# Optimization experiments

Hardware: AMD Instinct MI355X
Metric: run time of the kernel (lower is better)

## Reference

```python
import jax, jax.numpy as jnp
import numpy as np

N = 100000   # nodes
E = 400000   # edges (before self-loops)
G = 4000     # graphs in batch
F_IN = 32    # node_embedding
HID = 128    # hidden_channels
H = 3        # heads (hard-coded in module)
W3 = H * HID # 384, post-concat width
NC = 10      # num_classes
NL = 4       # num_layers
NEG_SLOPE = 0.2


def _lin(key, fan_in, fan_out):
    return jax.random.normal(key, (fan_in, fan_out), jnp.float32) * (1.0 / np.sqrt(fan_in))


def setup_inputs() -> dict:
    key = jax.random.key(0)
    ks = iter(jax.random.split(key, 40))
    x = jax.random.normal(next(ks), (N, F_IN), jnp.float32)
    edge_index = jax.random.randint(next(ks), (2, E), 0, N, dtype=jnp.int32)
    batch = jnp.sort(jax.random.randint(next(ks), (N,), 0, G, dtype=jnp.int32))
    inp = dict(x=x, edge_index=edge_index, batch=batch)
    # MLP stem
    inp['lin1_w'] = _lin(next(ks), F_IN, 2 * HID); inp['lin1_b'] = jnp.zeros((2 * HID,), jnp.float32)
    inp['lin2_w'] = _lin(next(ks), 2 * HID, HID);  inp['lin2_b'] = jnp.zeros((HID,), jnp.float32)
    # conv1: GATConv(HID -> HID, heads=3)
    inp['w0'] = _lin(next(ks), HID, W3)
    inp['as0'] = jax.random.normal(next(ks), (H, HID), jnp.float32) * 0.1
    inp['ad0'] = jax.random.normal(next(ks), (H, HID), jnp.float32) * 0.1
    inp['b0'] = jnp.zeros((W3,), jnp.float32)
    # remaining NL-1 convs: GATConv(W3 -> HID, heads=3), stacked
    inp['wl'] = jnp.stack([_lin(next(ks), W3, W3) for _ in range(NL - 1)])
    inp['asl'] = jax.random.normal(next(ks), (NL - 1, H, HID), jnp.float32) * 0.1
    inp['adl'] = jax.random.normal(next(ks), (NL - 1, H, HID), jnp.float32) * 0.1
    inp['bl'] = jnp.zeros((NL - 1, W3), jnp.float32)
    # batch norms (NL total, all width W3)
    inp['gamma'] = jnp.ones((NL, W3), jnp.float32)
    inp['beta'] = jnp.zeros((NL, W3), jnp.float32)
    # head
    inp['lin3_w'] = _lin(next(ks), W3, HID); inp['lin3_b'] = jnp.zeros((HID,), jnp.float32)
    inp['lin4_w'] = _lin(next(ks), HID, NC); inp['lin4_b'] = jnp.zeros((NC,), jnp.float32)
    return inp


def _gat(x, W, a_src, a_dst, bias, src, dst):
    # PyG GATConv, concat heads. x: [N, Fin]
    h = (x @ W).reshape(N, H, HID)                       # [N, H, C]
    es = jnp.einsum('nhc,hc->nh', h, a_src)              # [N, H]
    ed = jnp.einsum('nhc,hc->nh', h, a_dst)
    e = jax.nn.leaky_relu(es[src] + ed[dst], NEG_SLOPE)  # [Etot, H]
    m = jax.ops.segment_max(e, dst, num_segments=N)      # segment softmax over incoming edges
    p = jnp.exp(e - m[dst])
    s = jax.ops.segment_sum(p, dst, num_segments=N)
    alpha = p / s[dst]                                   # every node has a self-loop -> s>0
    out = jax.ops.segment_sum(alpha[:, :, None] * h[src], dst, num_segments=N)
    return out.reshape(N, W3) + bias


def _bn(x, g, b):
    mu = x.mean(0)
    var = x.var(0)
    return (x - mu) * jax.lax.rsqrt(var + 1e-5) * g + b


def reference(x, edge_index, batch, lin1_w, lin1_b, lin2_w, lin2_b,
              w0, as0, ad0, b0, wl, asl, adl, bl, gamma, beta,
              lin3_w, lin3_b, lin4_w, lin4_b):
    loop = jnp.arange(N, dtype=edge_index.dtype)
    src = jnp.concatenate([edge_index[0], loop])  # add_self_loops=True (PyG default)
    dst = jnp.concatenate([edge_index[1], loop])
    h = jax.nn.relu(x @ lin1_w + lin1_b)
    h = jax.nn.relu(h @ lin2_w + lin2_b)
    h = _gat(h, w0, as0, ad0, b0, src, dst)
    h = _bn(h, gamma[0], beta[0])
    for i in range(NL - 1):
        h = _gat(h, wl[i], asl[i], adl[i], bl[i], src, dst)
        h = _bn(h, gamma[i + 1], beta[i + 1])
    # global mean pool over graphs
    sums = jax.ops.segment_sum(h, batch, num_segments=G)
    cnt = jax.ops.segment_sum(jnp.ones((N,), h.dtype), batch, num_segments=G)
    g = sums / jnp.maximum(cnt, 1.0)[:, None]
    g = jax.nn.relu(g @ lin3_w + lin3_b)
    logits = g @ lin4_w + lin4_b
    return jax.nn.log_softmax(logits, axis=-1)
```

## Files before the change

kernel.cpp:

```cpp
#include <hip/hip_runtime.h>

#define NN      100000
#define NN2     100096
#define NE      400000
#define ETOT    500000
#define NG      4000
#define W3D     384
#define HIDD    128
#define NCLS    10
#define NSLICE  256

typedef unsigned short u16;
typedef unsigned int   u32;
typedef unsigned long long u64;
typedef __attribute__((ext_vector_type(8))) short short8;
typedef __attribute__((ext_vector_type(4))) float f32x4;

static __device__ __forceinline__ float bf2f(u16 u) {
  return __uint_as_float(((u32)u) << 16);
}
static __device__ __forceinline__ float bflo(u32 u) {
  return __uint_as_float(u << 16);
}
static __device__ __forceinline__ float bfhi(u32 u) {
  return __uint_as_float(u & 0xffff0000u);
}
static __device__ __forceinline__ u16 f2b(float f) {
  u32 u = __float_as_uint(f);
  u32 r = (u + 0x7fffu + ((u >> 16) & 1u)) >> 16;
  return (u16)r;
}

static __device__ __forceinline__ void llds16(const u16* g, u16* l) {
  __builtin_amdgcn_global_load_lds(
      (const __attribute__((address_space(1))) void*)(u64)(const void*)g,
      (__attribute__((address_space(3))) void*)(u64)(void*)l, 16, 0, 0);
}

#define WAITV0() asm volatile("s_waitcnt vmcnt(0)" ::: "memory")

__global__ void mg_zero_out(float* out, int n) {
  int i = blockIdx.x * 256 + threadIdx.x;
  if (i < n) out[i] = 0.f;
}

__global__ void mg_cvt_x(const float* __restrict__ x, u16* __restrict__ Xb) {
  int idx = blockIdx.x * 256 + threadIdx.x;
  if (idx >= NN2 * 64) return;
  int row = idx >> 6, col = idx & 63;
  Xb[idx] = (row < NN && col < 32) ? f2b(x[row * 32 + col]) : (u16)0;
}

__global__ void mg_transpose_pad(const float* __restrict__ in, u16* __restrict__ out,
                                 int K, int Nn, int Kpad) {
  int idx = blockIdx.x * 256 + threadIdx.x;
  if (idx >= Nn * Kpad) return;
  int n = idx / Kpad, kp = idx - n * Kpad;
  out[idx] = (kp < K) ? f2b(in[kp * Nn + n]) : (u16)0;
}

__global__ void mg_fold_w(const u16* __restrict__ Wt, const float* __restrict__ scale,
                          const float* __restrict__ shift, u16* __restrict__ Wp,
                          float* __restrict__ bp) {
  __shared__ float red[128];
  int j = blockIdx.x, t = threadIdx.x;
  const u16* src = Wt + (size_t)j * (W3D + 8);
  u16* dst = Wp + (size_t)j * (W3D + 8);
  float acc = 0.f;
  for (int kp = t; kp < W3D + 8; kp += 128) {
    int kt = (kp < W3D) ? kp : 0;
    float w = bf2f(src[kp]);
    dst[kp] = f2b(w * scale[kt]);
    acc += w * shift[kt];
  }
  red[t] = acc; __syncthreads();
  for (int off = 64; off; off >>= 1) {
    if (t < off) red[t] += red[t + off];
    __syncthreads();
  }
  if (t == 0) bp[j] = red[0];
}

__global__ void mg_edge_histo(const int* __restrict__ ei, int* __restrict__ deg) {
  int e = blockIdx.x * 256 + threadIdx.x;
  if (e >= ETOT) return;
  int d = (e < NE) ? ei[NE + e] : (e - NE);
  atomicAdd(&deg[d], 1);
}

__global__ void mg_scan1(const int* __restrict__ in, int* __restrict__ bsum, int n) {
  __shared__ int sd[256];
  int tid = threadIdx.x;
  int base = blockIdx.x * 1024 + tid * 4;
  int s = 0;
#pragma unroll
  for (int j = 0; j < 4; ++j) { int i = base + j; if (i < n) s += in[i]; }
  sd[tid] = s; __syncthreads();
  for (int off = 128; off > 0; off >>= 1) {
    if (tid < off) sd[tid] += sd[tid + off];
    __syncthreads();
  }
  if (tid == 0) bsum[blockIdx.x] = sd[0];
}

__global__ void mg_scan2(int* __restrict__ bsum, int nb) {
  __shared__ int sd[256];
  int tid = threadIdx.x;
  int v = (tid < nb) ? bsum[tid] : 0;
  sd[tid] = v; __syncthreads();
  for (int off = 1; off < 256; off <<= 1) {
    int t = (tid >= off) ? sd[tid - off] : 0;
    __syncthreads();
    sd[tid] += t;
    __syncthreads();
  }
  if (tid < nb) bsum[tid] = sd[tid] - v;
}

__global__ void mg_scan3(const int* __restrict__ in, const int* __restrict__ bexcl,
                         int* __restrict__ out, int n) {
  __shared__ int sd[256];
  int tid = threadIdx.x;
  int base = blockIdx.x * 1024 + tid * 4;
  int loc[4]; int s = 0;
#pragma unroll
  for (int j = 0; j < 4; ++j) { int i = base + j; loc[j] = (i < n) ? in[i] : 0; s += loc[j]; }
  sd[tid] = s; __syncthreads();
  for (int off = 1; off < 256; off <<= 1) {
    int t = (tid >= off) ? sd[tid - off] : 0;
    __syncthreads();
    sd[tid] += t;
    __syncthreads();
  }
  int run = sd[tid] - s + bexcl[blockIdx.x];
#pragma unroll
  for (int j = 0; j < 4; ++j) {
    int i = base + j;
    if (i < n) { out[i] = run; run += loc[j]; if (i == n - 1) out[n] = run; }
  }
}

__global__ void mg_edge_scatter(const int* __restrict__ ei, int* __restrict__ fill,
                                int* __restrict__ colsrc, int* __restrict__ dstc) {
  int e = blockIdx.x * 256 + threadIdx.x;
  if (e >= ETOT) return;
  int s, d;
  if (e < NE) { s = ei[e]; d = ei[NE + e]; } else { s = e - NE; d = s; }
  int pos = atomicAdd(&fill[d], 1);
  colsrc[pos] = s;
  dstc[pos] = d;
}

__global__ void mg_graph_ptr(const int* __restrict__ batch, int* __restrict__ gptr) {
  int g = blockIdx.x * 256 + threadIdx.x;
  if (g > NG) return;
  if (g == NG) { gptr[NG] = NN; return; }
  int lo = 0, hi = NN;
  while (lo < hi) { int mid = (lo + hi) >> 1; if (batch[mid] < g) lo = mid + 1; else hi = mid; }
  gptr[g] = lo;
}

__global__ __launch_bounds__(256) void mg_edge_p(
    const int* __restrict__ colsrc, const int* __restrict__ dstc,
    const float* __restrict__ es, const float* __restrict__ ed,
    float* __restrict__ pcsr) {
  int e = blockIdx.x * 256 + threadIdx.x;
  if (e >= ETOT) return;
  int s = colsrc[e], d = dstc[e];
  float4 a = *(const float4*)(es + 4 * s);
  float4 sd = *(const float4*)(es + 4 * d);
  float4 dd = *(const float4*)(ed + 4 * d);
  float4 p;
  {
    float ev = a.x + dd.x; ev = (ev > 0.f) ? ev : 0.2f * ev;
    float mv = sd.x + dd.x; mv = (mv > 0.f) ? mv : 0.2f * mv;
    p.x = __expf(ev - mv);
  }
  {
    float ev = a.y + dd.y; ev = (ev > 0.f) ? ev : 0.2f * ev;
    float mv = sd.y + dd.y; mv = (mv > 0.f) ? mv : 0.2f * mv;
    p.y = __expf(ev - mv);
  }
  {
    float ev = a.z + dd.z; ev = (ev > 0.f) ? ev : 0.2f * ev;
    float mv = sd.z + dd.z; mv = (mv > 0.f) ? mv : 0.2f * mv;
    p.z = __expf(ev - mv);
  }
  p.w = 0.f;
  *(float4*)(pcsr + (size_t)e * 4) = p;
}

#define CP 136

template<int K>
__global__ __launch_bounds__(512, 2) void mg_gemm(
    const u16* __restrict__ Ag, const u16* __restrict__ Bt,
    int MT, int Mstore, int Nn,
    u16* __restrict__ Cb, const float* __restrict__ bias, int relu,
    const float* __restrict__ asrc, const float* __restrict__ adst,
    float* __restrict__ aes, float* __restrict__ aed) {
  constexpr int KP = K + 8;
  constexpr int NITER = K / 32;
  constexpr int CSZ = (K == 384) ? 3 : ((K >= 128) ? 2 : 1);
  constexpr int CH = NITER / CSZ;
  static_assert(CH * CSZ == NITER && (CH & 1) == 0, "chunking");
  __shared__ u16 lds[128 * KP + 8 * 16 * CP];
  u16* Blds = lds;
  int tid = threadIdx.x;
  int lane = tid & 63, wv = tid >> 6;

  int gx = gridDim.x, gy = gridDim.y;
  int nwg = gx * gy;
  int lin = (int)blockIdx.y * gx + blockIdx.x;
  int q = nwg >> 3, r8 = nwg & 7;
  int xcd = lin & 7, sidx = lin >> 3;
  int nlin = (xcd < r8) ? (xcd * (q + 1) + sidx)
                        : (r8 * (q + 1) + (xcd - r8) * q + sidx);
  int mchunk = nlin / gy;
  int nidx = nlin - mchunk * gy;
  int n0 = nidx * 128;

  int lr = lane & 15, lq = lane >> 4;

  {
    const u16* Bg = Bt + (size_t)n0 * KP;
    constexpr int BBYTES = 128 * KP * 2;
    constexpr int FULL = BBYTES / 8192;
    constexpr int REMC = (BBYTES - FULL * 8192) / 16;
#pragma unroll
    for (int s = 0; s < FULL; ++s) {
      int off = s * 4096 + wv * 512 + lane * 8;
      llds16(Bg + off, Blds + off);
    }
    if (REMC > 0 && wv * 64 + lane < REMC) {
      int off = FULL * 4096 + wv * 512 + lane * 8;
      llds16(Bg + off, Blds + off);
    }
  }

  float bvv[8];
#pragma unroll
  for (int ni = 0; ni < 8; ++ni)
    bvv[ni] = bias ? bias[n0 + ni * 16 + lr] : 0.f;

  WAITV0();
  __syncthreads();

  u16* strip = lds + 128 * KP + wv * (16 * CP);

  int t0 = (int)(((long long)mchunk * MT) / gx);
  int t1 = (int)(((long long)(mchunk + 1) * MT) / gx);

  f32x4 acc[2][8];
  short8 bufE[2][CSZ], bufO[2][CSZ];

  auto loadCh = [&](short8 (&buf)[2][CSZ], int t, int ch) {
    const u16* Ar = Ag + (size_t)(t * 256 + wv * 32 + lr) * K + lq * 8 + ch * (CSZ * 32);
#pragma unroll
    for (int mi = 0; mi < 2; ++mi)
#pragma unroll
      for (int s = 0; s < CSZ; ++s)
        buf[mi][s] = *(const short8*)(Ar + (size_t)mi * 16 * K + s * 32);
  };
  auto compCh = [&](short8 (&buf)[2][CSZ], int ch) {
#pragma unroll
    for (int s = 0; s < CSZ; ++s) {
      int it = ch * CSZ + s;
      short8 bfr[8];
#pragma unroll
      for (int ni = 0; ni < 8; ++ni)
        bfr[ni] = *(const short8*)(Blds + (ni * 16 + lr) * KP + it * 32 + lq * 8);
#pragma unroll
      for (int mi = 0; mi < 2; ++mi)
#pragma unroll
        for (int ni = 0; ni < 8; ++ni)
          acc[mi][ni] = __builtin_amdgcn_mfma_f32_16x16x32_bf16(buf[mi][s], bfr[ni], acc[mi][ni], 0, 0, 0);
    }
  };

  loadCh(bufE, t0, 0);

  for (int t = t0; t < t1; ++t) {
    int rowbase = t * 256 + wv * 32;
#pragma unroll
    for (int mi = 0; mi < 2; ++mi)
#pragma unroll
      for (int ni = 0; ni < 8; ++ni) acc[mi][ni] = (f32x4){0.f, 0.f, 0.f, 0.f};

#pragma unroll
    for (int ch = 0; ch < CH; ch += 2) {
      loadCh(bufO, t, ch + 1);
      compCh(bufE, ch);
      if (ch + 2 < CH) loadCh(bufE, t, ch + 2);
      else if (t + 1 < t1) loadCh(bufE, t + 1, 0);
      compCh(bufO, ch + 1);
    }

#pragma unroll
    for (int mi = 0; mi < 2; ++mi) {
#pragma unroll
      for (int ni = 0; ni < 8; ++ni) {
#pragma unroll
        for (int r = 0; r < 4; ++r) {
          float v = acc[mi][ni][r] + bvv[ni];
          if (relu) v = fmaxf(v, 0.f);
          strip[(lq * 4 + r) * CP + ni * 16 + lr] = f2b(v);
        }
      }
      int row16 = lane >> 2, cb = lane & 3;
      const u16* src = strip + row16 * CP + cb * 32;
      uint4 c0 = *(const uint4*)(src);
      uint4 c1 = *(const uint4*)(src + 8);
      uint4 c2 = *(const uint4*)(src + 16);
      uint4 c3 = *(const uint4*)(src + 24);
      int mrow = rowbase + mi * 16 + row16;
      u16* gout = Cb + (size_t)mrow * Nn + n0 + cb * 32;
      *(uint4*)(gout)      = c0;
      *(uint4*)(gout + 8)  = c1;
      *(uint4*)(gout + 16) = c2;
      *(uint4*)(gout + 24) = c3;

      if (aes) {
        const float* ap = asrc + n0 + cb * 32;
        const float* dp = adst + n0 + cb * 32;
        float se = 0.f, de = 0.f;
        uint4 cj[4] = {c0, c1, c2, c3};
#pragma unroll
        for (int j = 0; j < 4; ++j) {
          float4 A0 = *(const float4*)(ap + j * 8);
          float4 A1 = *(const float4*)(ap + j * 8 + 4);
          float4 D0 = *(const float4*)(dp + j * 8);
          float4 D1 = *(const float4*)(dp + j * 8 + 4);
          uint4 rv = cj[j];
          float v0 = bflo(rv.x), v1 = bfhi(rv.x), v2 = bflo(rv.y), v3 = bfhi(rv.y);
          float v4 = bflo(rv.z), v5 = bfhi(rv.z), v6 = bflo(rv.w), v7 = bfhi(rv.w);
          se += v0 * A0.x + v1 * A0.y + v2 * A0.z + v3 * A0.w
              + v4 * A1.x + v5 * A1.y + v6 * A1.z + v7 * A1.w;
          de += v0 * D0.x + v1 * D0.y + v2 * D0.z + v3 * D0.w
              + v4 * D1.x + v5 * D1.y + v6 * D1.z + v7 * D1.w;
        }
        se += __shfl_xor(se, 1); se += __shfl_xor(se, 2);
        de += __shfl_xor(de, 1); de += __shfl_xor(de, 2);
        if (cb == 0 && mrow < Mstore) {
          aes[mrow * 4 + nidx] = se;
          aed[mrow * 4 + nidx] = de;
        }
      }
    }
  }
}

__global__ __launch_bounds__(256) void mg_aggregate(
    const u16* __restrict__ B, const float* __restrict__ pcsr,
    const int* __restrict__ rowptr, const int* __restrict__ colsrc,
    const float* __restrict__ bias,
    u16* __restrict__ A, float* __restrict__ stats) {
  __shared__ float bS[4 * W3D];
  __shared__ float bQ[4 * W3D];
  int wv = threadIdx.x >> 6, lane = threadIdx.x & 63;
  if (lane < 48) {
    int h = lane >> 4;
    int cc = lane * 8;
    float4 bv0 = *(const float4*)(bias + cc);
    float4 bv1 = *(const float4*)(bias + cc + 4);
    float stS[8], stQ[8];
#pragma unroll
    for (int j = 0; j < 8; ++j) { stS[j] = 0.f; stQ[j] = 0.f; }
#pragma unroll
    for (int sub = 0; sub < 2; ++sub) {
      int n = blockIdx.x * 8 + wv * 2 + sub;
      int r0 = rowptr[n], r1 = rowptr[n + 1];
      float accv[8];
#pragma unroll
      for (int j = 0; j < 8; ++j) accv[j] = 0.f;
      float ssum = 0.f;

      int   c0, c1, c2, c3, cb0, cb1, cb2, cb3;
      float p0, p1, p2, p3, pb0, pb1, pb2, pb3;
      uint4 v0, v1, v2, v3;

#define IDX_(CV, PV, RR) { int _i = ((RR) < r1) ? (RR) : (r1 - 1);          \
      CV = colsrc[_i]; PV = pcsr[(size_t)_i * 4 + h]; }
#define BLD_(VV, CV) { int _s = __builtin_amdgcn_readfirstlane(CV);         \
      VV = *(const uint4*)(B + (size_t)_s * W3D + cc); }
#define CMP_(PV, VV, RR) { float _pv = ((RR) < r1) ? PV : 0.f;              \
      ssum += _pv;                                                          \
      accv[0] += _pv * bflo(VV.x); accv[1] += _pv * bfhi(VV.x);             \
      accv[2] += _pv * bflo(VV.y); accv[3] += _pv * bfhi(VV.y);             \
      accv[4] += _pv * bflo(VV.z); accv[5] += _pv * bfhi(VV.z);             \
      accv[6] += _pv * bflo(VV.w); accv[7] += _pv * bfhi(VV.w); }

      IDX_(c0,  p0,  r0 + 0) IDX_(c1,  p1,  r0 + 1)
      IDX_(c2,  p2,  r0 + 2) IDX_(c3,  p3,  r0 + 3)
      IDX_(cb0, pb0, r0 + 4) IDX_(cb1, pb1, r0 + 5)
      IDX_(cb2, pb2, r0 + 6) IDX_(cb3, pb3, r0 + 7)
      BLD_(v0, c0) BLD_(v1, c1) BLD_(v2, c2) BLD_(v3, c3)

      for (int base = r0; base < r1; base += 4) {
        CMP_(p0, v0, base + 0)  BLD_(v0, cb0)
        CMP_(p1, v1, base + 1)  BLD_(v1, cb1)
        CMP_(p2, v2, base + 2)  BLD_(v2, cb2)
        CMP_(p3, v3, base + 3)  BLD_(v3, cb3)
        p0 = pb0; p1 = pb1; p2 = pb2; p3 = pb3;
        IDX_(cb0, pb0, base + 8)  IDX_(cb1, pb1, base + 9)
        IDX_(cb2, pb2, base + 10) IDX_(cb3, pb3, base + 11)
      }
#undef IDX_
#undef BLD_
#undef CMP_

      float inv = 1.0f / ssum;
      float v[8];
      v[0] = accv[0] * inv + bv0.x; v[1] = accv[1] * inv + bv0.y;
      v[2] = accv[2] * inv + bv0.z; v[3] = accv[3] * inv + bv0.w;
      v[4] = accv[4] * inv + bv1.x; v[5] = accv[5] * inv + bv1.y;
      v[6] = accv[6] * inv + bv1.z; v[7] = accv[7] * inv + bv1.w;
      uint4 st;
      st.x = (u32)f2b(v[0]) | ((u32)f2b(v[1]) << 16);
      st.y = (u32)f2b(v[2]) | ((u32)f2b(v[3]) << 16);
      st.z = (u32)f2b(v[4]) | ((u32)f2b(v[5]) << 16);
      st.w = (u32)f2b(v[6]) | ((u32)f2b(v[7]) << 16);
      *(uint4*)(A + (size_t)n * W3D + cc) = st;
#pragma unroll
      for (int j = 0; j < 8; ++j) { stS[j] += v[j]; stQ[j] += v[j] * v[j]; }
    }
    *(float4*)(bS + wv * W3D + cc)     = (float4){stS[0], stS[1], stS[2], stS[3]};
    *(float4*)(bS + wv * W3D + cc + 4) = (float4){stS[4], stS[5], stS[6], stS[7]};
    *(float4*)(bQ + wv * W3D + cc)     = (float4){stQ[0], stQ[1], stQ[2], stQ[3]};
    *(float4*)(bQ + wv * W3D + cc + 4) = (float4){stQ[4], stQ[5], stQ[6], stQ[7]};
  }
  __syncthreads();
  for (int t = threadIdx.x; t < W3D; t += 256) {
    float s = 0.f, q = 0.f;
#pragma unroll
    for (int w = 0; w < 4; ++w) { s += bS[w * W3D + t]; q += bQ[w * W3D + t]; }
    float* sl = stats + (size_t)(blockIdx.x & (NSLICE - 1)) * 768;
    atomicAdd(&sl[t], s);
    atomicAdd(&sl[W3D + t], q);
  }
}

__global__ void mg_bn_finalize(const float* __restrict__ stats, const float* __restrict__ gamma,
                               const float* __restrict__ beta, float* __restrict__ scale,
                               float* __restrict__ shift) {
  int c = threadIdx.x;
  float s = 0.f, q = 0.f;
  for (int b = 0; b < NSLICE; ++b) { s += stats[b * 768 + c]; q += stats[b * 768 + W3D + c]; }
  const float invN = 1.0f / (float)NN;
  float mu = s * invN;
  float var = fmaxf(q * invN - mu * mu, 0.f);
  float inv = rsqrtf(var + 1e-5f);
  float g = gamma[c], be = beta[c];
  scale[c] = g * inv;
  shift[c] = be - mu * g * inv;
}

__global__ void mg_pool(const u16* __restrict__ A, const float* __restrict__ scale,
                        const float* __restrict__ shift, const int* __restrict__ gptr,
                        float* __restrict__ pooled) {
  int g = blockIdx.x, c = threadIdx.x;
  int r0 = gptr[g], r1 = gptr[g + 1];
  float acc = 0.f;
  for (int n = r0; n < r1; ++n) acc += bf2f(A[(size_t)n * W3D + c]);
  int cnt = r1 - r0;
  float v = (cnt > 0) ? (acc / (float)cnt) * scale[c] + shift[c] : 0.f;
  pooled[g * W3D + c] = v;
}

__global__ void mg_head(const float* __restrict__ pooled, const float* __restrict__ w3,
                        const float* __restrict__ b3, const float* __restrict__ w4,
                        const float* __restrict__ b4, float* __restrict__ out) {
  __shared__ float p[W3D];
  __shared__ float g2[HIDD];
  __shared__ float lg[NCLS];
  int g = blockIdx.x, t = threadIdx.x;
  for (int i = t; i < W3D; i += 128) p[i] = pooled[g * W3D + i];
  __syncthreads();
  float acc = 0.f;
  for (int k = 0; k < W3D; ++k) acc += p[k] * w3[k * HIDD + t];
  g2[t] = fmaxf(acc + b3[t], 0.f);
  __syncthreads();
  if (t < NCLS) {
    float a = 0.f;
    for (int k = 0; k < HIDD; ++k) a += g2[k] * w4[k * NCLS + t];
    lg[t] = a + b4[t];
  }
  __syncthreads();
  if (t < NCLS) {
    float m = -1e30f;
#pragma unroll
    for (int j = 0; j < NCLS; ++j) m = fmaxf(m, lg[j]);
    float se = 0.f;
#pragma unroll
    for (int j = 0; j < NCLS; ++j) se += __expf(lg[j] - m);
    out[g * NCLS + t] = lg[t] - m - __logf(se);
  }
}

extern "C" void kernel_launch(void* const* d_in, const int* in_sizes, int n_in,
                              void* d_out, int out_size, void* d_ws, size_t ws_size,
                              hipStream_t stream) {
  const float* x     = (const float*)d_in[0];
  const int*   ei    = (const int*)d_in[1];
  const int*   batch = (const int*)d_in[2];
  const float* w1    = (const float*)d_in[3];
  const float* b1    = (const float*)d_in[4];
  const float* w2    = (const float*)d_in[5];
  const float* b2    = (const float*)d_in[6];
  const float* w0    = (const float*)d_in[7];
  const float* as0   = (const float*)d_in[8];
  const float* ad0   = (const float*)d_in[9];
  const float* b0    = (const float*)d_in[10];
  const float* wl    = (const float*)d_in[11];
  const float* asl   = (const float*)d_in[12];
  const float* adl   = (const float*)d_in[13];
  const float* bl    = (const float*)d_in[14];
  const float* gamma = (const float*)d_in[15];
  const float* beta  = (const float*)d_in[16];
  const float* w3    = (const float*)d_in[17];
  const float* b3    = (const float*)d_in[18];
  const float* w4    = (const float*)d_in[19];
  const float* b4    = (const float*)d_in[20];
  float* out = (float*)d_out;

  char* w = (char*)d_ws;
  auto alloc = [&](size_t bytes) -> void* {
    void* p = (void*)w;
    w += (bytes + 255) & ~(size_t)255;
    return p;
  };
  u16*   P      = (u16*)alloc((size_t)NN2 * W3D * 2);
  u16*   Q      = (u16*)alloc((size_t)NN2 * W3D * 2);
  float* es     = (float*)alloc((size_t)NN * 4 * 4);
  float* ed     = (float*)alloc((size_t)NN * 4 * 4);
  int*   deg    = (int*)alloc((size_t)NN * 4);
  int*   rowptr = (int*)alloc((size_t)(NN + 1) * 4);
  int*   fill   = (int*)alloc((size_t)NN * 4);
  int*   colsrc = (int*)alloc((size_t)ETOT * 4);
  int*   dstc   = (int*)alloc((size_t)ETOT * 4);
  float* pcsr   = (float*)alloc((size_t)ETOT * 4 * 4);
  int*   bsum   = (int*)alloc(256 * 4);
  float* stats  = (float*)alloc((size_t)NSLICE * 768 * 4);
  float* scale  = (float*)alloc(W3D * 4);
  float* shift  = (float*)alloc(W3D * 4);
  float* bprime = (float*)alloc(W3D * 4);
  int*   gptr   = (int*)alloc((size_t)(NG + 1) * 4);
  float* pooled = (float*)alloc((size_t)NG * W3D * 4);
  u16*   W1T    = (u16*)alloc((size_t)256 * 72 * 2);
  u16*   W2T    = (u16*)alloc((size_t)128 * 264 * 2);
  u16*   W0T    = (u16*)alloc((size_t)384 * 136 * 2);
  u16*   WlT    = (u16*)alloc((size_t)3 * 384 * 392 * 2);
  u16*   WpT    = (u16*)alloc((size_t)384 * 392 * 2);
  u16*   Xb     = Q;

  if ((size_t)(w - (char*)d_ws) > ws_size) {
    mg_zero_out<<<(out_size + 255) / 256, 256, 0, stream>>>(out, out_size);
    return;
  }

  mg_cvt_x<<<(NN2 * 64 + 255) / 256, 256, 0, stream>>>(x, Xb);
  mg_transpose_pad<<<(256 * 72 + 255) / 256, 256, 0, stream>>>(w1, W1T, 32, 256, 72);
  mg_transpose_pad<<<(128 * 264 + 255) / 256, 256, 0, stream>>>(w2, W2T, 256, 128, 264);
  mg_transpose_pad<<<(384 * 136 + 255) / 256, 256, 0, stream>>>(w0, W0T, 128, 384, 136);
  for (int i = 0; i < 3; ++i)
    mg_transpose_pad<<<(384 * 392 + 255) / 256, 256, 0, stream>>>(
        wl + (size_t)i * 384 * 384, WlT + (size_t)i * 384 * 392, 384, 384, 392);

  hipMemsetAsync(deg, 0, (size_t)NN * 4, stream);
  mg_edge_histo<<<(ETOT + 255) / 256, 256, 0, stream>>>(ei, deg);
  int nb = (NN + 1023) / 1024;
  mg_scan1<<<nb, 256, 0, stream>>>(deg, bsum, NN);
  mg_scan2<<<1, 256, 0, stream>>>(bsum, nb);
  mg_scan3<<<nb, 256, 0, stream>>>(deg, bsum, rowptr, NN);
  hipMemcpyAsync(fill, rowptr, (size_t)NN * 4, hipMemcpyDeviceToDevice, stream);
  mg_edge_scatter<<<(ETOT + 255) / 256, 256, 0, stream>>>(ei, fill, colsrc, dstc);
  mg_graph_ptr<<<(NG + 1 + 255) / 256, 256, 0, stream>>>(batch, gptr);

  dim3 blk(512);
  const int MT = NN2 / 256;
  const int EPB = (ETOT + 255) / 256;

  mg_gemm<64><<<dim3(128, 2), blk, 0, stream>>>(Xb, W1T, MT, NN, 256,
                                                P, b1, 1,
                                                nullptr, nullptr, nullptr, nullptr);
  mg_gemm<256><<<dim3(256, 1), blk, 0, stream>>>(P, W2T, MT, NN, 128,
                                                 Q, b2, 1,
                                                 nullptr, nullptr, nullptr, nullptr);

  for (int i = 0; i < 4; ++i) {
    const float* bi_g = nullptr;
    const u16* Bt;
    if (i == 0) {
      Bt = W0T;
    } else {
      mg_fold_w<<<384, 128, 0, stream>>>(WlT + (size_t)(i - 1) * 384 * 392,
                                         scale, shift, WpT, bprime);
      Bt = WpT;
      bi_g = bprime;
    }
    const float* as = (i == 0) ? as0 : (asl + (size_t)(i - 1) * 384);
    const float* ad = (i == 0) ? ad0 : (adl + (size_t)(i - 1) * 384);
    const float* bi = (i == 0) ? b0  : (bl  + (size_t)(i - 1) * 384);
    hipMemsetAsync(stats, 0, (size_t)NSLICE * 768 * 4, stream);
    if (i == 0)
      mg_gemm<128><<<dim3(85, 3), blk, 0, stream>>>(Q, Bt, MT, NN, W3D,
                                                    P, bi_g, 0,
                                                    as, ad, es, ed);
    else
      mg_gemm<384><<<dim3(85, 3), blk, 0, stream>>>(Q, Bt, MT, NN, W3D,
                                                    P, bi_g, 0,
                                                    as, ad, es, ed);
    mg_edge_p<<<EPB, 256, 0, stream>>>(colsrc, dstc, es, ed, pcsr);
    mg_aggregate<<<NN / 8, 256, 0, stream>>>(P, pcsr, rowptr, colsrc, bi, Q, stats);
    mg_bn_finalize<<<1, 384, 0, stream>>>(stats, gamma + (size_t)i * W3D,
                                          beta + (size_t)i * W3D, scale, shift);
  }

  mg_pool<<<NG, 384, 0, stream>>>(Q, scale, shift, gptr, pooled);
  mg_head<<<NG, 128, 0, stream>>>(pooled, w3, b3, w4, b4, out);
}
```

Before: 972.0 us.

## Raise MFMA wave priority, parallelize BN finalize, hoist stats memset

Three independent tweaks. The GEMM inner loop wraps its MFMA burst in s_setprio to favour math issue over loads from other waves. The BN finalize kernel moves from one block of 384 threads looping over 256 slices to 6 blocks whose 4 thread groups split the slice reduction and combine through shared memory. The per-layer stats memset is replaced by one upfront memset of a 4x larger buffer with a per-layer offset, which removes three memset launches and adds a little workspace.

```diff
diff --git a/kernel.cpp b/kernel.cpp
--- a/kernel.cpp
+++ b/kernel.cpp
@@ -270,11 +270,13 @@
 #pragma unroll
       for (int ni = 0; ni < 8; ++ni)
         bfr[ni] = *(const short8*)(Blds + (ni * 16 + lr) * KP + it * 32 + lq * 8);
+      __builtin_amdgcn_s_setprio(1);
 #pragma unroll
       for (int mi = 0; mi < 2; ++mi)
 #pragma unroll
         for (int ni = 0; ni < 8; ++ni)
           acc[mi][ni] = __builtin_amdgcn_mfma_f32_16x16x32_bf16(buf[mi][s], bfr[ni], acc[mi][ni], 0, 0, 0);
+      __builtin_amdgcn_s_setprio(0);
     }
   };
 
@@ -301,10 +303,10 @@
 #pragma unroll
       for (int ni = 0; ni < 8; ++ni) {
 #pragma unroll
-        for (int r = 0; r < 4; ++r) {
-          float v = acc[mi][ni][r] + bvv[ni];
+        for (int r2 = 0; r2 < 4; ++r2) {
+          float v = acc[mi][ni][r2] + bvv[ni];
           if (relu) v = fmaxf(v, 0.f);
-          strip[(lq * 4 + r) * CP + ni * 16 + lr] = f2b(v);
+          strip[(lq * 4 + r2) * CP + ni * 16 + lr] = f2b(v);
         }
       }
       int row16 = lane >> 2, cb = lane & 3;
@@ -443,16 +445,29 @@
 __global__ void mg_bn_finalize(const float* __restrict__ stats, const float* __restrict__ gamma,
                                const float* __restrict__ beta, float* __restrict__ scale,
                                float* __restrict__ shift) {
-  int c = threadIdx.x;
+  __shared__ float rs[4][64];
+  __shared__ float rq[4][64];
+  int cl = threadIdx.x & 63;
+  int part = threadIdx.x >> 6;
+  int c = blockIdx.x * 64 + cl;
   float s = 0.f, q = 0.f;
-  for (int b = 0; b < NSLICE; ++b) { s += stats[b * 768 + c]; q += stats[b * 768 + W3D + c]; }
-  const float invN = 1.0f / (float)NN;
-  float mu = s * invN;
-  float var = fmaxf(q * invN - mu * mu, 0.f);
-  float inv = rsqrtf(var + 1e-5f);
-  float g = gamma[c], be = beta[c];
-  scale[c] = g * inv;
-  shift[c] = be - mu * g * inv;
+  for (int b = part * 64; b < part * 64 + 64; ++b) {
+    s += stats[b * 768 + c];
+    q += stats[b * 768 + W3D + c];
+  }
+  rs[part][cl] = s; rq[part][cl] = q;
+  __syncthreads();
+  if (part == 0) {
+    s = rs[0][cl] + rs[1][cl] + rs[2][cl] + rs[3][cl];
+    q = rq[0][cl] + rq[1][cl] + rq[2][cl] + rq[3][cl];
+    const float invN = 1.0f / (float)NN;
+    float mu = s * invN;
+    float var = fmaxf(q * invN - mu * mu, 0.f);
+    float inv = rsqrtf(var + 1e-5f);
+    float g = gamma[c], be = beta[c];
+    scale[c] = g * inv;
+    shift[c] = be - mu * g * inv;
+  }
 }
 
 __global__ void mg_pool(const u16* __restrict__ A, const float* __restrict__ scale,
@@ -540,7 +555,7 @@
   int*   dstc   = (int*)alloc((size_t)ETOT * 4);
   float* pcsr   = (float*)alloc((size_t)ETOT * 4 * 4);
   int*   bsum   = (int*)alloc(256 * 4);
-  float* stats  = (float*)alloc((size_t)NSLICE * 768 * 4);
+  float* stats  = (float*)alloc((size_t)4 * NSLICE * 768 * 4);
   float* scale  = (float*)alloc(W3D * 4);
   float* shift  = (float*)alloc(W3D * 4);
   float* bprime = (float*)alloc(W3D * 4);
@@ -557,6 +572,8 @@
     mg_zero_out<<<(out_size + 255) / 256, 256, 0, stream>>>(out, out_size);
     return;
   }
+
+  hipMemsetAsync(stats, 0, (size_t)4 * NSLICE * 768 * 4, stream);
 
   mg_cvt_x<<<(NN2 * 64 + 255) / 256, 256, 0, stream>>>(x, Xb);
   mg_transpose_pad<<<(256 * 72 + 255) / 256, 256, 0, stream>>>(w1, W1T, 32, 256, 72);
@@ -601,7 +618,7 @@
     const float* as = (i == 0) ? as0 : (asl + (size_t)(i - 1) * 384);
     const float* ad = (i == 0) ? ad0 : (adl + (size_t)(i - 1) * 384);
     const float* bi = (i == 0) ? b0  : (bl  + (size_t)(i - 1) * 384);
-    hipMemsetAsync(stats, 0, (size_t)NSLICE * 768 * 4, stream);
+    float* st_i = stats + (size_t)i * NSLICE * 768;
     if (i == 0)
       mg_gemm<128><<<dim3(85, 3), blk, 0, stream>>>(Q, Bt, MT, NN, W3D,
                                                     P, bi_g, 0,
@@ -611,8 +628,8 @@
                                                     P, bi_g, 0,
                                                     as, ad, es, ed);
     mg_edge_p<<<EPB, 256, 0, stream>>>(colsrc, dstc, es, ed, pcsr);
-    mg_aggregate<<<NN / 8, 256, 0, stream>>>(P, pcsr, rowptr, colsrc, bi, Q, stats);
-    mg_bn_finalize<<<1, 384, 0, stream>>>(stats, gamma + (size_t)i * W3D,
+    mg_aggregate<<<NN / 8, 256, 0, stream>>>(P, pcsr, rowptr, colsrc, bi, Q, st_i);
+    mg_bn_finalize<<<6, 256, 0, stream>>>(st_i, gamma + (size_t)i * W3D,
                                           beta + (size_t)i * W3D, scale, shift);
   }
 
```

After: 986.5 us. No clear change (+1.5%).
